# Kernel optimization log

Measured on AMD Instinct MI355X. Metric: run time of the kernel, lower is better.

The kernel has to match this reference:

```python
import jax, jax.numpy as jnp
import numpy as np

DIM = 128

def setup_inputs() -> dict:
    key = jax.random.key(0)
    ks = jax.random.split(key, 5)
    B, N, C = 4096, 64, DIM
    x = jax.random.normal(ks[0], (B, N, C), dtype=jnp.float32)
    w_qkv = jax.random.normal(ks[1], (C, 3 * C), dtype=jnp.float32) / np.sqrt(C)
    b_qkv = jax.random.normal(ks[2], (3 * C,), dtype=jnp.float32) * 0.01
    w_proj = jax.random.normal(ks[3], (C, C), dtype=jnp.float32) / np.sqrt(C)
    b_proj = jax.random.normal(ks[4], (C,), dtype=jnp.float32) * 0.01
    return {"x": x, "w_qkv": w_qkv, "b_qkv": b_qkv, "w_proj": w_proj, "b_proj": b_proj}

def reference(x, w_qkv, b_qkv, w_proj, b_proj):
    B, N, C = x.shape
    qkv = x @ w_qkv + b_qkv                      # [B,N,3C]
    q, k, v = jnp.split(qkv, 3, axis=-1)         # each [B,N,C]
    attn = jnp.einsum('bnc,bmc->bnm', q, k) * (C ** -0.5)
    attn = jax.nn.softmax(attn, axis=-1)
    out = jnp.einsum('bnm,bmc->bnc', attn, v)
    return out @ w_proj + b_proj
```

## Files before the change

kernel.cpp:

```cpp
#include <hip/hip_runtime.h>

using bf16x8 = __attribute__((ext_vector_type(8))) short;
using f32x4  = __attribute__((ext_vector_type(4))) float;

__device__ __forceinline__ unsigned short f2bf(float f) {
  unsigned u = __builtin_bit_cast(unsigned, f);
  u += 0x7fffu + ((u >> 16) & 1u);
  return (unsigned short)(u >> 16);
}

__global__ __launch_bounds__(128) void prep_weights(
    const float* __restrict__ wqkv, const float* __restrict__ bqkv,
    const float* __restrict__ wproj, const float* __restrict__ bproj,
    void* __restrict__ ws) {
  __shared__ float W[128][129];
  unsigned short* wsu = (unsigned short*)ws;
  float* wsF = (float*)ws;
  const int tid = threadIdx.x;
  const int cp = blockIdx.x & 127;
  const bool second = blockIdx.x >= 128;
  const int off = second ? 256 : 0;
  for (int r = 0; r < 128; ++r)
    W[r][tid] = wqkv[r * 384 + off + tid];
  __syncthreads();
  float acc = 0.f;
  #pragma unroll 8
  for (int o = 0; o < 128; ++o) {
    float bc = second ? wproj[o * 128 + cp] : wqkv[cp * 384 + 128 + o];
    acc += W[tid][o] * bc;
  }
  wsu[(second ? 16384 : 0) + cp * 128 + tid] = f2bf(acc);
  if (tid == 0) {
    float a2 = 0.f;
    if (!second) {
      for (int o = 0; o < 128; ++o) a2 += wqkv[cp * 384 + 128 + o] * bqkv[o];
      wsF[16384 + cp] = a2;
    } else {
      for (int o = 0; o < 128; ++o) a2 += bqkv[256 + o] * wproj[o * 128 + cp];
      wsF[16512 + cp] = a2 + bproj[cp];
    }
  }
}

__global__ __launch_bounds__(256, 4) void win_attn(
    const float* __restrict__ x, const void* __restrict__ ws,
    float* __restrict__ out) {
  __shared__ unsigned short sX[8192];
  __shared__ unsigned short sT[8192];
  const unsigned short* MB  = (const unsigned short*)ws;
  const unsigned short* W2B = MB + 16384;
  const float* v2 = (const float*)((const char*)ws + 65536);
  const float* b2 = v2 + 128;

  const int tid  = threadIdx.x;
  const int wave = tid >> 6;
  const int lane = tid & 63;
  const int g    = lane >> 4;
  const int lr   = lane & 15;
  const float* xb = x + (size_t)blockIdx.x * 8192;
  const float scale = 0.08838834764831845f;
  const float l2e   = 1.4426950408889634f;

  #pragma unroll
  for (int i = 0; i < 8; ++i) {
    int e = tid + 256 * i;
    float4 v = ((const float4*)xb)[e];
    int r = e >> 5, c4 = (e & 31) * 4;
    ushort4 pk = make_ushort4(f2bf(v.x), f2bf(v.y), f2bf(v.z), f2bf(v.w));
    *(ushort4*)&sX[r * 128 + (c4 ^ ((r & 7) << 3))] = pk;
  }
  __syncthreads();

  float wacc = 0.f;
  {
    const int r = 16 * wave + lr;
    #pragma unroll
    for (int ii = 0; ii < 4; ++ii) {
      int c0 = 32 * g + 8 * ii;
      bf16x8 f = *(const bf16x8*)&sX[r * 128 + (c0 ^ ((r & 7) << 3))];
      #pragma unroll
      for (int e2 = 0; e2 < 8; ++e2) {
        float xf = __builtin_bit_cast(float, ((unsigned)(unsigned short)f[e2]) << 16);
        wacc += xf * v2[c0 + e2];
      }
    }
    wacc += __shfl_xor(wacc, 16, 64);
    wacc += __shfl_xor(wacc, 32, 64);
  }
  const float uu = exp2f(wacc * (scale * l2e));

  f32x4 accT[8];
  #pragma unroll
  for (int ct = 0; ct < 8; ++ct) accT[ct] = f32x4{0.f,0.f,0.f,0.f};
  {
    const int ra = 16 * wave + lr;
    #pragma unroll
    for (int k0 = 0; k0 < 128; k0 += 32) {
      bf16x8 a = *(const bf16x8*)&sX[ra * 128 + ((k0 + 8 * g) ^ ((ra & 7) << 3))];
      #pragma unroll
      for (int ct = 0; ct < 8; ++ct) {
        bf16x8 bv = *(const bf16x8*)&MB[(16 * ct + lr) * 128 + k0 + 8 * g];
        accT[ct] = __builtin_amdgcn_mfma_f32_16x16x32_bf16(a, bv, accT[ct], 0, 0, 0);
      }
    }
  }
  #pragma unroll
  for (int ct = 0; ct < 8; ++ct)
    #pragma unroll
    for (int j = 0; j < 4; ++j) {
      int r = 16 * wave + 4 * g + j, c = 16 * ct + lr;
      sT[r * 128 + (c ^ ((r & 7) << 3))] = f2bf(accT[ct][j]);
    }

  f32x4 s[4];
  #pragma unroll
  for (int ct = 0; ct < 4; ++ct) s[ct] = f32x4{0.f,0.f,0.f,0.f};
  {
    const int ra = 16 * wave + lr;
    #pragma unroll
    for (int k0 = 0; k0 < 128; k0 += 32) {
      bf16x8 a = *(const bf16x8*)&sT[ra * 128 + ((k0 + 8 * g) ^ ((ra & 7) << 3))];
      #pragma unroll
      for (int ct = 0; ct < 4; ++ct) {
        int rb = 16 * ct + lr;
        bf16x8 bv = *(const bf16x8*)&sX[rb * 128 + ((k0 + 8 * g) ^ ((rb & 7) << 3))];
        s[ct] = __builtin_amdgcn_mfma_f32_16x16x32_bf16(a, bv, s[ct], 0, 0, 0);
      }
    }
  }
  #pragma unroll
  for (int j = 0; j < 4; ++j) {
    float mm = fmaxf(fmaxf(s[0][j], s[1][j]), fmaxf(s[2][j], s[3][j]));
    #pragma unroll
    for (int off = 1; off < 16; off <<= 1) mm = fmaxf(mm, __shfl_xor(mm, off, 64));
    const int r = 16 * wave + 4 * g + j;
    #pragma unroll
    for (int ct = 0; ct < 4; ++ct) {
      float p = exp2f((s[ct][j] - mm) * (scale * l2e));
      sT[r * 128 + ((16 * ct + lr) ^ ((r & 7) << 3))] = f2bf(p);
    }
  }

  f32x4 z[8];
  #pragma unroll
  for (int ct = 0; ct < 8; ++ct) z[ct] = f32x4{0.f,0.f,0.f,0.f};
  {
    const int ra = 16 * wave + lr;
    #pragma unroll
    for (int k0 = 0; k0 < 128; k0 += 32) {
      bf16x8 a = *(const bf16x8*)&sX[ra * 128 + ((k0 + 8 * g) ^ ((ra & 7) << 3))];
      #pragma unroll
      for (int ct = 0; ct < 8; ++ct) {
        bf16x8 bv = *(const bf16x8*)&W2B[(16 * ct + lr) * 128 + k0 + 8 * g];
        z[ct] = __builtin_amdgcn_mfma_f32_16x16x32_bf16(a, bv, z[ct], 0, 0, 0);
      }
    }
  }
  __syncthreads();

  {
    const int m0 = 16 * wave + 4 * g;
    float u4[4];
    #pragma unroll
    for (int j = 0; j < 4; ++j) u4[j] = __shfl(uu, 4 * g + j, 64);
    #pragma unroll
    for (int ct = 0; ct < 8; ++ct) {
      const int c = 16 * ct + lr;
      ushort4 pk = make_ushort4(f2bf(z[ct][0] * u4[0]), f2bf(z[ct][1] * u4[1]),
                                f2bf(z[ct][2] * u4[2]), f2bf(z[ct][3] * u4[3]));
      if (ct < 4) *(ushort4*)&sT[c * 128 + 64 + (m0 ^ ((c & 7) << 3))] = pk;
      else        *(ushort4*)&sX[(c - 64) * 128 + (m0 ^ ((c & 7) << 3))] = pk;
    }
    if (g == 0) sX[64 + 16 * wave + lr] = f2bf(uu);
  }
  __syncthreads();

  f32x4 y[8], y8;
  #pragma unroll
  for (int ct = 0; ct < 8; ++ct) y[ct] = f32x4{0.f,0.f,0.f,0.f};
  y8 = f32x4{0.f,0.f,0.f,0.f};
  {
    const int ra = 16 * wave + lr;
    #pragma unroll
    for (int k0 = 0; k0 < 64; k0 += 32) {
      const int mk = k0 + 8 * g;
      bf16x8 a = *(const bf16x8*)&sT[ra * 128 + (mk ^ ((ra & 7) << 3))];
      #pragma unroll
      for (int ct = 0; ct < 8; ++ct) {
        const int c = 16 * ct + lr;
        bf16x8 bv = (ct < 4)
          ? *(const bf16x8*)&sT[c * 128 + 64 + (mk ^ ((c & 7) << 3))]
          : *(const bf16x8*)&sX[(c - 64) * 128 + (mk ^ ((c & 7) << 3))];
        y[ct] = __builtin_amdgcn_mfma_f32_16x16x32_bf16(a, bv, y[ct], 0, 0, 0);
      }
      bf16x8 uv = *(const bf16x8*)&sX[64 + mk];
      y8 = __builtin_amdgcn_mfma_f32_16x16x32_bf16(a, uv, y8, 0, 0, 0);
    }
  }
  float* ob = out + (size_t)blockIdx.x * 8192;
  float rs4[4];
  #pragma unroll
  for (int j = 0; j < 4; ++j) rs4[j] = 1.0f / y8[j];
  #pragma unroll
  for (int ct = 0; ct < 8; ++ct) {
    const int c = 16 * ct + lr;
    const float bb = b2[c];
    #pragma unroll
    for (int j = 0; j < 4; ++j) {
      int r = 16 * wave + 4 * g + j;
      ob[r * 128 + c] = y[ct][j] * rs4[j] + bb;
    }
  }
}

extern "C" void kernel_launch(void* const* d_in, const int* in_sizes, int n_in,
                              void* d_out, int out_size, void* d_ws, size_t ws_size,
                              hipStream_t stream) {
  const float* x     = (const float*)d_in[0];
  const float* wqkv  = (const float*)d_in[1];
  const float* bqkv  = (const float*)d_in[2];
  const float* wproj = (const float*)d_in[3];
  const float* bproj = (const float*)d_in[4];
  float* out = (float*)d_out;

  prep_weights<<<256, 128, 0, stream>>>(wqkv, bqkv, wproj, bproj, d_ws);
  win_attn<<<4096, 256, 0, stream>>>(x, d_ws, out);
}
```

Measured before the change: 372.0 us.

## Process four windows per block with register prefetch of next window

Each block now loops over four consecutive windows instead of one and launches a quarter as many blocks. While the current window is computed, the next window's x is loaded in two halves into registers, packed to bf16, and written into shared memory after the current window finishes. The aim is to hide global load latency behind MFMA work and to amortise block launch cost. The price is more live registers (xr, xb), which may reduce occupancy, plus two extra barriers per window, and a smaller grid of 1024 blocks.

```diff
diff --git a/kernel.cpp b/kernel.cpp
--- a/kernel.cpp
+++ b/kernel.cpp
@@ -7,6 +7,9 @@
   unsigned u = __builtin_bit_cast(unsigned, f);
   u += 0x7fffu + ((u >> 16) & 1u);
   return (unsigned short)(u >> 16);
+}
+__device__ __forceinline__ unsigned pk2(float a, float b) {
+  return (unsigned)f2bf(a) | ((unsigned)f2bf(b) << 16);
 }
 
 __global__ __launch_bounds__(128) void prep_weights(
@@ -57,158 +60,207 @@
   const int lane = tid & 63;
   const int g    = lane >> 4;
   const int lr   = lane & 15;
-  const float* xb = x + (size_t)blockIdx.x * 8192;
-  const float scale = 0.08838834764831845f;
-  const float l2e   = 1.4426950408889634f;
-
-  #pragma unroll
-  for (int i = 0; i < 8; ++i) {
-    int e = tid + 256 * i;
-    float4 v = ((const float4*)xb)[e];
-    int r = e >> 5, c4 = (e & 31) * 4;
-    ushort4 pk = make_ushort4(f2bf(v.x), f2bf(v.y), f2bf(v.z), f2bf(v.w));
-    *(ushort4*)&sX[r * 128 + (c4 ^ ((r & 7) << 3))] = pk;
+  const float sl2e = 0.08838834764831845f * 1.4426950408889634f;
+
+  const size_t w0 = (size_t)blockIdx.x * 4;
+
+  {
+    const float* xb0 = x + w0 * 8192;
+    #pragma unroll
+    for (int i = 0; i < 8; ++i) {
+      int e = tid + 256 * i;
+      float4 v = ((const float4*)xb0)[e];
+      int r = e >> 5, c4 = (e & 31) * 4;
+      *(uint2*)&sX[r * 128 + (c4 ^ ((r & 7) << 3))] =
+          make_uint2(pk2(v.x, v.y), pk2(v.z, v.w));
+    }
   }
   __syncthreads();
 
-  float wacc = 0.f;
-  {
-    const int r = 16 * wave + lr;
-    #pragma unroll
-    for (int ii = 0; ii < 4; ++ii) {
-      int c0 = 32 * g + 8 * ii;
-      bf16x8 f = *(const bf16x8*)&sX[r * 128 + (c0 ^ ((r & 7) << 3))];
-      #pragma unroll
-      for (int e2 = 0; e2 < 8; ++e2) {
-        float xf = __builtin_bit_cast(float, ((unsigned)(unsigned short)f[e2]) << 16);
-        wacc += xf * v2[c0 + e2];
-      }
-    }
-    wacc += __shfl_xor(wacc, 16, 64);
-    wacc += __shfl_xor(wacc, 32, 64);
-  }
-  const float uu = exp2f(wacc * (scale * l2e));
-
-  f32x4 accT[8];
-  #pragma unroll
-  for (int ct = 0; ct < 8; ++ct) accT[ct] = f32x4{0.f,0.f,0.f,0.f};
-  {
-    const int ra = 16 * wave + lr;
-    #pragma unroll
-    for (int k0 = 0; k0 < 128; k0 += 32) {
-      bf16x8 a = *(const bf16x8*)&sX[ra * 128 + ((k0 + 8 * g) ^ ((ra & 7) << 3))];
+  unsigned xr[16];
+  float4 xb[4];
+
+  #pragma unroll 1
+  for (int win = 0; win < 4; ++win) {
+    const bool pref = (win < 3);
+    const float* xn = x + (w0 + win + 1) * 8192;
+
+    if (pref) {
+      #pragma unroll
+      for (int i = 0; i < 4; ++i) xb[i] = ((const float4*)xn)[tid + 256 * i];
+    }
+
+    float wacc = 0.f;
+    {
+      const int r = 16 * wave + lr;
+      #pragma unroll
+      for (int ii = 0; ii < 4; ++ii) {
+        int c0 = 32 * g + 8 * ii;
+        bf16x8 f = *(const bf16x8*)&sX[r * 128 + (c0 ^ ((r & 7) << 3))];
+        #pragma unroll
+        for (int e2 = 0; e2 < 8; ++e2) {
+          float xf = __builtin_bit_cast(float, ((unsigned)(unsigned short)f[e2]) << 16);
+          wacc += xf * v2[c0 + e2];
+        }
+      }
+      wacc += __shfl_xor(wacc, 16, 64);
+      wacc += __shfl_xor(wacc, 32, 64);
+    }
+    const float uu = exp2f(wacc * sl2e);
+
+    f32x4 accT[8];
+    #pragma unroll
+    for (int ct = 0; ct < 8; ++ct) accT[ct] = f32x4{0.f,0.f,0.f,0.f};
+    {
+      const int ra = 16 * wave + lr;
+      #pragma unroll
+      for (int k0 = 0; k0 < 128; k0 += 32) {
+        bf16x8 a = *(const bf16x8*)&sX[ra * 128 + ((k0 + 8 * g) ^ ((ra & 7) << 3))];
+        #pragma unroll
+        for (int ct = 0; ct < 8; ++ct) {
+          bf16x8 bv = *(const bf16x8*)&MB[(16 * ct + lr) * 128 + k0 + 8 * g];
+          accT[ct] = __builtin_amdgcn_mfma_f32_16x16x32_bf16(a, bv, accT[ct], 0, 0, 0);
+        }
+      }
+    }
+    #pragma unroll
+    for (int ct = 0; ct < 8; ++ct)
+      #pragma unroll
+      for (int j = 0; j < 4; ++j) {
+        int r = 16 * wave + 4 * g + j, c = 16 * ct + lr;
+        sT[r * 128 + (c ^ ((r & 7) << 3))] = f2bf(accT[ct][j]);
+      }
+
+    if (pref) {
+      #pragma unroll
+      for (int i = 0; i < 4; ++i) {
+        xr[2 * i]     = pk2(xb[i].x, xb[i].y);
+        xr[2 * i + 1] = pk2(xb[i].z, xb[i].w);
+      }
+    }
+
+    f32x4 s[4];
+    #pragma unroll
+    for (int ct = 0; ct < 4; ++ct) s[ct] = f32x4{0.f,0.f,0.f,0.f};
+    {
+      const int ra = 16 * wave + lr;
+      #pragma unroll
+      for (int k0 = 0; k0 < 128; k0 += 32) {
+        bf16x8 a = *(const bf16x8*)&sT[ra * 128 + ((k0 + 8 * g) ^ ((ra & 7) << 3))];
+        #pragma unroll
+        for (int ct = 0; ct < 4; ++ct) {
+          int rb = 16 * ct + lr;
+          bf16x8 bv = *(const bf16x8*)&sX[rb * 128 + ((k0 + 8 * g) ^ ((rb & 7) << 3))];
+          s[ct] = __builtin_amdgcn_mfma_f32_16x16x32_bf16(a, bv, s[ct], 0, 0, 0);
+        }
+      }
+    }
+    #pragma unroll
+    for (int j = 0; j < 4; ++j) {
+      float mm = fmaxf(fmaxf(s[0][j], s[1][j]), fmaxf(s[2][j], s[3][j]));
+      #pragma unroll
+      for (int off = 1; off < 16; off <<= 1) mm = fmaxf(mm, __shfl_xor(mm, off, 64));
+      const int r = 16 * wave + 4 * g + j;
+      #pragma unroll
+      for (int ct = 0; ct < 4; ++ct) {
+        float p = exp2f((s[ct][j] - mm) * sl2e);
+        sT[r * 128 + ((16 * ct + lr) ^ ((r & 7) << 3))] = f2bf(p);
+      }
+    }
+
+    if (pref) {
+      #pragma unroll
+      for (int i = 0; i < 4; ++i) xb[i] = ((const float4*)xn)[tid + 256 * (4 + i)];
+    }
+
+    f32x4 z[8];
+    #pragma unroll
+    for (int ct = 0; ct < 8; ++ct) z[ct] = f32x4{0.f,0.f,0.f,0.f};
+    {
+      const int ra = 16 * wave + lr;
+      #pragma unroll
+      for (int k0 = 0; k0 < 128; k0 += 32) {
+        bf16x8 a = *(const bf16x8*)&sX[ra * 128 + ((k0 + 8 * g) ^ ((ra & 7) << 3))];
+        #pragma unroll
+        for (int ct = 0; ct < 8; ++ct) {
+          bf16x8 bv = *(const bf16x8*)&W2B[(16 * ct + lr) * 128 + k0 + 8 * g];
+          z[ct] = __builtin_amdgcn_mfma_f32_16x16x32_bf16(a, bv, z[ct], 0, 0, 0);
+        }
+      }
+    }
+    __syncthreads();
+
+    {
+      const int m0 = 16 * wave + 4 * g;
+      float u4[4];
+      #pragma unroll
+      for (int j = 0; j < 4; ++j) u4[j] = __shfl(uu, 4 * g + j, 64);
       #pragma unroll
       for (int ct = 0; ct < 8; ++ct) {
-        bf16x8 bv = *(const bf16x8*)&MB[(16 * ct + lr) * 128 + k0 + 8 * g];
-        accT[ct] = __builtin_amdgcn_mfma_f32_16x16x32_bf16(a, bv, accT[ct], 0, 0, 0);
-      }
-    }
-  }
-  #pragma unroll
-  for (int ct = 0; ct < 8; ++ct)
-    #pragma unroll
-    for (int j = 0; j < 4; ++j) {
-      int r = 16 * wave + 4 * g + j, c = 16 * ct + lr;
-      sT[r * 128 + (c ^ ((r & 7) << 3))] = f2bf(accT[ct][j]);
-    }
-
-  f32x4 s[4];
-  #pragma unroll
-  for (int ct = 0; ct < 4; ++ct) s[ct] = f32x4{0.f,0.f,0.f,0.f};
-  {
-    const int ra = 16 * wave + lr;
-    #pragma unroll
-    for (int k0 = 0; k0 < 128; k0 += 32) {
-      bf16x8 a = *(const bf16x8*)&sT[ra * 128 + ((k0 + 8 * g) ^ ((ra & 7) << 3))];
-      #pragma unroll
-      for (int ct = 0; ct < 4; ++ct) {
-        int rb = 16 * ct + lr;
-        bf16x8 bv = *(const bf16x8*)&sX[rb * 128 + ((k0 + 8 * g) ^ ((rb & 7) << 3))];
-        s[ct] = __builtin_amdgcn_mfma_f32_16x16x32_bf16(a, bv, s[ct], 0, 0, 0);
-      }
-    }
-  }
-  #pragma unroll
-  for (int j = 0; j < 4; ++j) {
-    float mm = fmaxf(fmaxf(s[0][j], s[1][j]), fmaxf(s[2][j], s[3][j]));
-    #pragma unroll
-    for (int off = 1; off < 16; off <<= 1) mm = fmaxf(mm, __shfl_xor(mm, off, 64));
-    const int r = 16 * wave + 4 * g + j;
-    #pragma unroll
-    for (int ct = 0; ct < 4; ++ct) {
-      float p = exp2f((s[ct][j] - mm) * (scale * l2e));
-      sT[r * 128 + ((16 * ct + lr) ^ ((r & 7) << 3))] = f2bf(p);
-    }
-  }
-
-  f32x4 z[8];
-  #pragma unroll
-  for (int ct = 0; ct < 8; ++ct) z[ct] = f32x4{0.f,0.f,0.f,0.f};
-  {
-    const int ra = 16 * wave + lr;
-    #pragma unroll
-    for (int k0 = 0; k0 < 128; k0 += 32) {
-      bf16x8 a = *(const bf16x8*)&sX[ra * 128 + ((k0 + 8 * g) ^ ((ra & 7) << 3))];
-      #pragma unroll
-      for (int ct = 0; ct < 8; ++ct) {
-        bf16x8 bv = *(const bf16x8*)&W2B[(16 * ct + lr) * 128 + k0 + 8 * g];
-        z[ct] = __builtin_amdgcn_mfma_f32_16x16x32_bf16(a, bv, z[ct], 0, 0, 0);
-      }
-    }
-  }
-  __syncthreads();
-
-  {
-    const int m0 = 16 * wave + 4 * g;
-    float u4[4];
-    #pragma unroll
-    for (int j = 0; j < 4; ++j) u4[j] = __shfl(uu, 4 * g + j, 64);
+        const int c = 16 * ct + lr;
+        ushort4 pk = make_ushort4(f2bf(z[ct][0] * u4[0]), f2bf(z[ct][1] * u4[1]),
+                                  f2bf(z[ct][2] * u4[2]), f2bf(z[ct][3] * u4[3]));
+        if (ct < 4) *(ushort4*)&sT[c * 128 + 64 + (m0 ^ ((c & 7) << 3))] = pk;
+        else        *(ushort4*)&sX[(c - 64) * 128 + (m0 ^ ((c & 7) << 3))] = pk;
+      }
+      if (g == 0) sX[64 + 16 * wave + lr] = f2bf(uu);
+    }
+
+    if (pref) {
+      #pragma unroll
+      for (int i = 0; i < 4; ++i) {
+        xr[8 + 2 * i] = pk2(xb[i].x, xb[i].y);
+        xr[9 + 2 * i] = pk2(xb[i].z, xb[i].w);
+      }
+    }
+    __syncthreads();
+
+    f32x4 y[8], y8;
+    #pragma unroll
+    for (int ct = 0; ct < 8; ++ct) y[ct] = f32x4{0.f,0.f,0.f,0.f};
+    y8 = f32x4{0.f,0.f,0.f,0.f};
+    {
+      const int ra = 16 * wave + lr;
+      #pragma unroll
+      for (int k0 = 0; k0 < 64; k0 += 32) {
+        const int mk = k0 + 8 * g;
+        bf16x8 a = *(const bf16x8*)&sT[ra * 128 + (mk ^ ((ra & 7) << 3))];
+        #pragma unroll
+        for (int ct = 0; ct < 8; ++ct) {
+          const int c = 16 * ct + lr;
+          bf16x8 bv = (ct < 4)
+            ? *(const bf16x8*)&sT[c * 128 + 64 + (mk ^ ((c & 7) << 3))]
+            : *(const bf16x8*)&sX[(c - 64) * 128 + (mk ^ ((c & 7) << 3))];
+          y[ct] = __builtin_amdgcn_mfma_f32_16x16x32_bf16(a, bv, y[ct], 0, 0, 0);
+        }
+        bf16x8 uv = *(const bf16x8*)&sX[64 + mk];
+        y8 = __builtin_amdgcn_mfma_f32_16x16x32_bf16(a, uv, y8, 0, 0, 0);
+      }
+    }
+    float* ob = out + (size_t)(w0 + win) * 8192;
+    float rs4[4];
+    #pragma unroll
+    for (int j = 0; j < 4; ++j) rs4[j] = 1.0f / y8[j];
     #pragma unroll
     for (int ct = 0; ct < 8; ++ct) {
       const int c = 16 * ct + lr;
-      ushort4 pk = make_ushort4(f2bf(z[ct][0] * u4[0]), f2bf(z[ct][1] * u4[1]),
-                                f2bf(z[ct][2] * u4[2]), f2bf(z[ct][3] * u4[3]));
-      if (ct < 4) *(ushort4*)&sT[c * 128 + 64 + (m0 ^ ((c & 7) << 3))] = pk;
-      else        *(ushort4*)&sX[(c - 64) * 128 + (m0 ^ ((c & 7) << 3))] = pk;
-    }
-    if (g == 0) sX[64 + 16 * wave + lr] = f2bf(uu);
-  }
-  __syncthreads();
-
-  f32x4 y[8], y8;
-  #pragma unroll
-  for (int ct = 0; ct < 8; ++ct) y[ct] = f32x4{0.f,0.f,0.f,0.f};
-  y8 = f32x4{0.f,0.f,0.f,0.f};
-  {
-    const int ra = 16 * wave + lr;
-    #pragma unroll
-    for (int k0 = 0; k0 < 64; k0 += 32) {
-      const int mk = k0 + 8 * g;
-      bf16x8 a = *(const bf16x8*)&sT[ra * 128 + (mk ^ ((ra & 7) << 3))];
-      #pragma unroll
-      for (int ct = 0; ct < 8; ++ct) {
-        const int c = 16 * ct + lr;
-        bf16x8 bv = (ct < 4)
-          ? *(const bf16x8*)&sT[c * 128 + 64 + (mk ^ ((c & 7) << 3))]
-          : *(const bf16x8*)&sX[(c - 64) * 128 + (mk ^ ((c & 7) << 3))];
-        y[ct] = __builtin_amdgcn_mfma_f32_16x16x32_bf16(a, bv, y[ct], 0, 0, 0);
-      }
-      bf16x8 uv = *(const bf16x8*)&sX[64 + mk];
-      y8 = __builtin_amdgcn_mfma_f32_16x16x32_bf16(a, uv, y8, 0, 0, 0);
-    }
-  }
-  float* ob = out + (size_t)blockIdx.x * 8192;
-  float rs4[4];
-  #pragma unroll
-  for (int j = 0; j < 4; ++j) rs4[j] = 1.0f / y8[j];
-  #pragma unroll
-  for (int ct = 0; ct < 8; ++ct) {
-    const int c = 16 * ct + lr;
-    const float bb = b2[c];
-    #pragma unroll
-    for (int j = 0; j < 4; ++j) {
-      int r = 16 * wave + 4 * g + j;
-      ob[r * 128 + c] = y[ct][j] * rs4[j] + bb;
+      const float bb = b2[c];
+      #pragma unroll
+      for (int j = 0; j < 4; ++j) {
+        int r = 16 * wave + 4 * g + j;
+        ob[r * 128 + c] = y[ct][j] * rs4[j] + bb;
+      }
+    }
+
+    if (pref) {
+      __syncthreads();
+      #pragma unroll
+      for (int i = 0; i < 8; ++i) {
+        int e = tid + 256 * i;
+        int r = e >> 5, c4 = (e & 31) * 4;
+        *(uint2*)&sX[r * 128 + (c4 ^ ((r & 7) << 3))] = make_uint2(xr[2 * i], xr[2 * i + 1]);
+      }
+      __syncthreads();
     }
   }
 }
@@ -224,5 +276,5 @@
   float* out = (float*)d_out;
 
   prep_weights<<<256, 128, 0, stream>>>(wqkv, bqkv, wproj, bproj, d_ws);
-  win_attn<<<4096, 256, 0, stream>>>(x, d_ws, out);
-}
+  win_attn<<<1024, 256, 0, stream>>>(x, d_ws, out);
+}
```

Result: slower. 745.2 us (+100.3%).
